# Kernel optimization log

Measured on AMD Instinct MI355X. Metric: run time of the kernel, lower is better.

Reference implementation:

```python
import jax, jax.numpy as jnp
import numpy as np

NUM_HEADS = 12
DILATIONS = (1, 2, 4)
POOL_STRIDE = 2
LINFORMER_SEQ = 128


def setup_inputs() -> dict:
    key = jax.random.key(0)
    ks = jax.random.split(key, 8)
    B, N, C = 32, 1024, 768
    bank = 64
    return {
        "x": jax.random.normal(ks[0], (B, N, C), jnp.float32),
        "Wqkv": jax.random.normal(ks[1], (C, 3 * C), jnp.float32) * 0.02,
        "bqkv": jnp.zeros((3 * C,), jnp.float32),
        "E_k": jax.random.normal(ks[2], (LINFORMER_SEQ, 64), jnp.float32) * 0.02,
        "E_v": jax.random.normal(ks[3], (LINFORMER_SEQ, 64), jnp.float32) * 0.02,
        "Wproj": jax.random.normal(ks[4], (C, C), jnp.float32) * 0.02,
        "bproj": jnp.zeros((C,), jnp.float32),
        "k_bank": jax.random.normal(ks[5], (B, bank, C), jnp.float32),
        "v_bank": jax.random.normal(ks[6], (B, bank, C), jnp.float32),
    }


def reference(x, Wqkv, bqkv, E_k, E_v, Wproj, bproj, k_bank, v_bank):
    B, N, C = x.shape
    H = NUM_HEADS
    D = C // H
    S = int(np.sqrt(N))  # spatial side, N must be a perfect square

    # multi-scale dilated token gather
    xg = x.reshape(B, S, S, C)
    multi = [xg[:, ::d, ::d, :].reshape(B, -1, C) for d in DILATIONS]
    xm = jnp.concatenate(multi, axis=1)  # (B, NM, C)

    # landmark average pooling (kernel=stride=POOL_STRIDE, no padding)
    NM = xm.shape[1]
    NP = NM // POOL_STRIDE
    xp = xm[:, : NP * POOL_STRIDE].reshape(B, NP, POOL_STRIDE, C).mean(axis=2)

    # qkv on pooled landmarks, keep k and v heads
    qkv_p = (xp @ Wqkv + bqkv).reshape(B, NP, 3, H, D)
    k = qkv_p[:, :, 1].transpose(0, 2, 1, 3)  # (B,H,NP,D)
    v = qkv_p[:, :, 2].transpose(0, 2, 1, 3)

    # truncate/pad to Linformer seq_len (here NP=672 > 128 -> truncate)
    if k.shape[2] < LINFORMER_SEQ:
        pad = LINFORMER_SEQ - k.shape[2]
        k = jnp.pad(k, ((0, 0), (0, 0), (0, pad), (0, 0)))
        v = jnp.pad(v, ((0, 0), (0, 0), (0, pad), (0, 0)))
    else:
        k = k[:, :, :LINFORMER_SEQ]
        v = v[:, :, :LINFORMER_SEQ]

    # Linformer low-rank compression: E.T @ k
    kc = jnp.einsum('sc,bhsd->bhcd', E_k, k)  # (B,H,64,D)
    vc = jnp.einsum('sc,bhsd->bhcd', E_v, v)

    # memory bank heads
    kb = k_bank.reshape(B, -1, H, D).transpose(0, 2, 1, 3)
    vb = v_bank.reshape(B, -1, H, D).transpose(0, 2, 1, 3)
    k_full = jnp.concatenate([kc, kb], axis=2)  # (B,H,128,D)
    v_full = jnp.concatenate([vc, vb], axis=2)

    # queries from full-resolution tokens
    q = (x @ Wqkv + bqkv).reshape(B, N, 3, H, D)[:, :, 0].transpose(0, 2, 1, 3)

    # scaled dot-product attention (dropout p=0 in eval / reference)
    scale = 1.0 / jnp.sqrt(jnp.asarray(D, x.dtype))
    scores = jnp.einsum('bhqd,bhkd->bhqk', q, k_full) * scale
    attn = jax.nn.softmax(scores, axis=-1)
    out = jnp.einsum('bhqk,bhkd->bhqd', attn, v_full)

    out = out.transpose(0, 2, 1, 3).reshape(B, N, C)
    return out @ Wproj + bproj
```

## Files before the change

kernel.cpp:

```cpp
#include <hip/hip_runtime.h>

#define BB    32
#define NSEQ  1024
#define CDIM  768
#define NH    12
#define HD    64
#define LKEYS 128
#define NPOOL 128

typedef __bf16 bf16x8 __attribute__((ext_vector_type(8)));
typedef float  f32x4  __attribute__((ext_vector_type(4)));

__device__ __forceinline__ ushort f2bf(float f) {
    union { float f; uint u; } v; v.f = f;
    uint u = v.u;
    uint r = u + 0x7FFFu + ((u >> 16) & 1u);
    return (ushort)(r >> 16);
}
__device__ __forceinline__ uint pack2(float x, float y) {
    return (uint)f2bf(x) | ((uint)f2bf(y) << 16);
}

__global__ __launch_bounds__(256) void cvt_bf16_kernel(const float* __restrict__ src,
                                                       ushort* __restrict__ dst, int n8)
{
    int idx = blockIdx.x * 256 + threadIdx.x;
    if (idx >= n8) return;
    float4 a = ((const float4*)src)[idx * 2];
    float4 b = ((const float4*)src)[idx * 2 + 1];
    uint4 o;
    o.x = pack2(a.x, a.y); o.y = pack2(a.z, a.w);
    o.z = pack2(b.x, b.y); o.w = pack2(b.z, b.w);
    ((uint4*)dst)[idx] = o;
}

__global__ __launch_bounds__(256) void transpose_cvt_kernel(const float* __restrict__ src,
                                                            ushort* __restrict__ dst,
                                                            int R, int C)
{
    __shared__ ushort tile[32][33];
    int bc = blockIdx.x * 32, br = blockIdx.y * 32;
    int tx = threadIdx.x & 31, ty = threadIdx.x >> 5;
#pragma unroll
    for (int i = 0; i < 32; i += 8)
        tile[ty + i][tx] = f2bf(src[(size_t)(br + ty + i) * C + bc + tx]);
    __syncthreads();
#pragma unroll
    for (int i = 0; i < 32; i += 8)
        dst[(size_t)(bc + ty + i) * R + br + tx] = tile[tx][ty + i];
}

__global__ __launch_bounds__(256) void pool_kernel(const float* __restrict__ x,
                                                   ushort* __restrict__ xp)
{
    int idx = blockIdx.x * 256 + threadIdx.x;
    int c8 = idx % 96;
    int t  = idx / 96;
    int i  = t % NPOOL;
    int b  = t / NPOOL;
    if (b >= BB) return;
    const float4* x4 = (const float4*)x;
    size_t base0 = ((size_t)(b * NSEQ + 2 * i)) * 192 + c8 * 2;
    size_t base1 = base0 + 192;
    float4 a0 = x4[base0], a1 = x4[base0 + 1];
    float4 b0 = x4[base1], b1 = x4[base1 + 1];
    uint4 o;
    o.x = pack2(0.5f * (a0.x + b0.x), 0.5f * (a0.y + b0.y));
    o.y = pack2(0.5f * (a0.z + b0.z), 0.5f * (a0.w + b0.w));
    o.z = pack2(0.5f * (a1.x + b1.x), 0.5f * (a1.y + b1.y));
    o.w = pack2(0.5f * (a1.z + b1.z), 0.5f * (a1.w + b1.w));
    ((uint4*)xp)[idx] = o;
}

template <bool OBF16>
__global__ __launch_bounds__(256) void mfma_gemm_kernel(
    const ushort* __restrict__ A, const ushort* __restrict__ Bt,
    const float* __restrict__ bias, void* __restrict__ Cout,
    int M, int N, int K)
{
    __shared__ ushort As[128 * 32];
    __shared__ ushort Bs[128 * 32];

    int tid  = threadIdx.x;
    int wave = tid >> 6, lane = tid & 63;

    int nwg  = gridDim.x * gridDim.y;
    int bid  = blockIdx.y * gridDim.x + blockIdx.x;
    int q    = nwg >> 3, r = nwg & 7;
    int xcd  = bid & 7, j = bid >> 3;
    int flat = (xcd < r ? xcd * (q + 1) : r * (q + 1) + (xcd - r) * q) + j;
    int n0 = (flat % gridDim.x) * 128;
    int m0 = (flat / gridDim.x) * 128;

    int wm = wave >> 1, wn = wave & 1;
    int lm = lane & 15, lh = lane >> 4;

    f32x4 acc[4][4] = {};

    for (int k0 = 0; k0 < K; k0 += 32) {
        __syncthreads();
#pragma unroll
        for (int t = 0; t < 2; t++) {
            int fl = wave * 128 + t * 64 + lane;
            int row = fl >> 2, kc = (fl & 3) * 8;
            const ushort* gA = A  + (size_t)(m0 + row) * K + k0 + kc;
            const ushort* gB = Bt + (size_t)(n0 + row) * K + k0 + kc;
            __builtin_amdgcn_global_load_lds(
                (const __attribute__((address_space(1))) void*)gA,
                (__attribute__((address_space(3))) void*)(As + (size_t)(wave * 128 + t * 64) * 8),
                16, 0, 0);
            __builtin_amdgcn_global_load_lds(
                (const __attribute__((address_space(1))) void*)gB,
                (__attribute__((address_space(3))) void*)(Bs + (size_t)(wave * 128 + t * 64) * 8),
                16, 0, 0);
        }
        __syncthreads();

        bf16x8 af[4], bfr[4];
#pragma unroll
        for (int i = 0; i < 4; i++)
            af[i] = *(const bf16x8*)((const void*)&As[(wm * 64 + i * 16 + lm) * 32 + lh * 8]);
#pragma unroll
        for (int jj = 0; jj < 4; jj++)
            bfr[jj] = *(const bf16x8*)((const void*)&Bs[(wn * 64 + jj * 16 + lm) * 32 + lh * 8]);
#pragma unroll
        for (int i = 0; i < 4; i++)
#pragma unroll
            for (int jj = 0; jj < 4; jj++)
                acc[i][jj] = __builtin_amdgcn_mfma_f32_16x16x32_bf16(af[i], bfr[jj], acc[i][jj], 0, 0, 0);
    }

    int crow = m0 + wm * 64, ccol = n0 + wn * 64;
#pragma unroll
    for (int jj = 0; jj < 4; jj++) {
        int col = ccol + jj * 16 + lm;
        float bb = bias[col];
        if constexpr (OBF16) {
            ushort* C = (ushort*)Cout;
#pragma unroll
            for (int i = 0; i < 4; i++)
#pragma unroll
                for (int rr = 0; rr < 4; rr++)
                    C[(size_t)(crow + i * 16 + lh * 4 + rr) * N + col] = f2bf(acc[i][jj][rr] + bb);
        } else {
            float* C = (float*)Cout;
#pragma unroll
            for (int i = 0; i < 4; i++)
#pragma unroll
                for (int rr = 0; rr < 4; rr++)
                    C[(size_t)(crow + i * 16 + lh * 4 + rr) * N + col] = acc[i][jj][rr] + bb;
        }
    }
}

__global__ __launch_bounds__(256) void compress_kernel(
    const float* __restrict__ kvp,
    const float* __restrict__ Ek, const float* __restrict__ Ev,
    const float* __restrict__ kbank, const float* __restrict__ vbank,
    ushort* __restrict__ kfull, ushort* __restrict__ vfullT)
{
    __shared__ float Es[128 * 64];
    __shared__ float Sl[128 * 64];

    int tid = threadIdx.x;
    int h = blockIdx.x, b = blockIdx.y, which = blockIdx.z;
    const float* E    = which ? Ev : Ek;
    const float* bank = which ? vbank : kbank;

#pragma unroll
    for (int i = 0; i < 8; i++) {
        int flat = tid + i * 256;
        *(float4*)&Es[flat * 4] = *(const float4*)&E[flat * 4];
    }
    const float* src = kvp + (size_t)b * 128 * 1536 + which * 768 + h * HD;
#pragma unroll
    for (int i = 0; i < 8; i++) {
        int flat = tid + i * 256;
        int s = flat >> 4, d4 = flat & 15;
        *(float4*)&Sl[s * 64 + d4 * 4] = *(const float4*)&src[(size_t)s * 1536 + d4 * 4];
    }

    const float* bankbase = bank + (size_t)b * 64 * CDIM + h * HD;
    ushort* outK = kfull  + (size_t)(b * NH + h) * LKEYS * HD;
    ushort* outV = vfullT + (size_t)(b * NH + h) * HD * LKEYS;

#pragma unroll
    for (int i = 0; i < 4; i++) {
        int flat = tid + i * 256;
        int j = flat >> 4, d4 = flat & 15;
        float4 v = *(const float4*)&bankbase[(size_t)j * CDIM + d4 * 4];
        if (!which) {
            ushort4 o;
            o.x = f2bf(v.x); o.y = f2bf(v.y); o.z = f2bf(v.z); o.w = f2bf(v.w);
            *(ushort4*)&outK[(size_t)(64 + j) * HD + d4 * 4] = o;
        } else {
            outV[(size_t)(d4 * 4 + 0) * LKEYS + 64 + j] = f2bf(v.x);
            outV[(size_t)(d4 * 4 + 1) * LKEYS + 64 + j] = f2bf(v.y);
            outV[(size_t)(d4 * 4 + 2) * LKEYS + 64 + j] = f2bf(v.z);
            outV[(size_t)(d4 * 4 + 3) * LKEYS + 64 + j] = f2bf(v.w);
        }
    }
    __syncthreads();

    int tx = tid & 15, ty = tid >> 4;
    float acc[4][4];
#pragma unroll
    for (int i = 0; i < 4; i++)
#pragma unroll
        for (int j = 0; j < 4; j++) acc[i][j] = 0.f;

#pragma unroll 4
    for (int s = 0; s < 128; s++) {
        float4 av = *(const float4*)&Es[s * 64 + ty * 4];
        float4 bv = *(const float4*)&Sl[s * 64 + tx * 4];
        float a[4] = {av.x, av.y, av.z, av.w};
        float bb[4] = {bv.x, bv.y, bv.z, bv.w};
#pragma unroll
        for (int i = 0; i < 4; i++)
#pragma unroll
            for (int j = 0; j < 4; j++)
                acc[i][j] += a[i] * bb[j];
    }
    if (!which) {
#pragma unroll
        for (int i = 0; i < 4; i++) {
            ushort4 o;
            o.x = f2bf(acc[i][0]); o.y = f2bf(acc[i][1]);
            o.z = f2bf(acc[i][2]); o.w = f2bf(acc[i][3]);
            *(ushort4*)&outK[(size_t)(ty * 4 + i) * HD + tx * 4] = o;
        }
    } else {
#pragma unroll
        for (int i = 0; i < 4; i++)
#pragma unroll
            for (int j = 0; j < 4; j++)
                outV[(size_t)(tx * 4 + j) * LKEYS + ty * 4 + i] = f2bf(acc[i][j]);
    }
}

__global__ __launch_bounds__(256) void attn_mfma_kernel(
    const ushort* __restrict__ qb, const ushort* __restrict__ kf,
    const ushort* __restrict__ vt, ushort* __restrict__ ob)
{
    __shared__ __align__(16) ushort lds[64 * 72 + 128 * 72 + 64 * 136];
    ushort* Qs = lds;
    ushort* Ks = lds + 64 * 72;
    ushort* Vs = lds + 64 * 72 + 128 * 72;
    ushort* Ps = lds;

    int tid  = threadIdx.x;
    int wave = tid >> 6, lane = tid & 63;
    int lm = lane & 15, lh = lane >> 4;
    int qt = blockIdx.x, h = blockIdx.y, b = blockIdx.z;

    const ushort* qbase = qb + ((size_t)(b * NSEQ + qt * 64)) * CDIM + h * HD;
    const ushort* kbase = kf + (size_t)(b * NH + h) * LKEYS * HD;
    const ushort* vbase = vt + (size_t)(b * NH + h) * HD * LKEYS;

#pragma unroll
    for (int it = 0; it < 2; it++) {
        int flat = tid + it * 256;
        int row = flat >> 3, seg = flat & 7;
        *(uint4*)&Qs[row * 72 + seg * 8] = *(const uint4*)&qbase[(size_t)row * CDIM + seg * 8];
    }
#pragma unroll
    for (int it = 0; it < 4; it++) {
        int flat = tid + it * 256;
        int row = flat >> 3, seg = flat & 7;
        *(uint4*)&Ks[row * 72 + seg * 8] = *(const uint4*)&kbase[(size_t)row * HD + seg * 8];
    }
#pragma unroll
    for (int it = 0; it < 4; it++) {
        int flat = tid + it * 256;
        int row = flat >> 4, seg = flat & 15;
        *(uint4*)&Vs[row * 136 + seg * 8] = *(const uint4*)&vbase[(size_t)row * LKEYS + seg * 8];
    }
    __syncthreads();

    f32x4 sacc[8] = {};
    bf16x8 aq[2];
#pragma unroll
    for (int ks = 0; ks < 2; ks++)
        aq[ks] = *(const bf16x8*)((const void*)&Qs[(wave * 16 + lm) * 72 + ks * 32 + lh * 8]);
#pragma unroll
    for (int j = 0; j < 8; j++)
#pragma unroll
        for (int ks = 0; ks < 2; ks++) {
            bf16x8 bk = *(const bf16x8*)((const void*)&Ks[(j * 16 + lm) * 72 + ks * 32 + lh * 8]);
            sacc[j] = __builtin_amdgcn_mfma_f32_16x16x32_bf16(aq[ks], bk, sacc[j], 0, 0, 0);
        }

    float rinv[4];
#pragma unroll
    for (int r = 0; r < 4; r++) {
        float m = sacc[0][r];
#pragma unroll
        for (int j = 1; j < 8; j++) m = fmaxf(m, sacc[j][r]);
#pragma unroll
        for (int off = 1; off < 16; off <<= 1) m = fmaxf(m, __shfl_xor(m, off, 64));
        float s = 0.f;
#pragma unroll
        for (int j = 0; j < 8; j++) {
            float e = __expf((sacc[j][r] - m) * 0.125f);
            sacc[j][r] = e;
            s += e;
        }
#pragma unroll
        for (int off = 1; off < 16; off <<= 1) s += __shfl_xor(s, off, 64);
        rinv[r] = 1.f / s;
    }

    __syncthreads();
#pragma unroll
    for (int j = 0; j < 8; j++)
#pragma unroll
        for (int r = 0; r < 4; r++)
            Ps[(size_t)(wave * 16 + lh * 4 + r) * 136 + j * 16 + lm] = f2bf(sacc[j][r] * rinv[r]);
    __syncthreads();

    f32x4 oacc[4] = {};
#pragma unroll
    for (int ks = 0; ks < 4; ks++) {
        bf16x8 ap = *(const bf16x8*)((const void*)&Ps[(wave * 16 + lm) * 136 + ks * 32 + lh * 8]);
#pragma unroll
        for (int j = 0; j < 4; j++) {
            bf16x8 bv = *(const bf16x8*)((const void*)&Vs[(j * 16 + lm) * 136 + ks * 32 + lh * 8]);
            oacc[j] = __builtin_amdgcn_mfma_f32_16x16x32_bf16(ap, bv, oacc[j], 0, 0, 0);
        }
    }

    ushort* obase = ob + ((size_t)(b * NSEQ + qt * 64)) * CDIM + h * HD;
#pragma unroll
    for (int j = 0; j < 4; j++)
#pragma unroll
        for (int r = 0; r < 4; r++)
            obase[(size_t)(wave * 16 + lh * 4 + r) * CDIM + j * 16 + lm] = f2bf(oacc[j][r]);
}

extern "C" void kernel_launch(void* const* d_in, const int* in_sizes, int n_in,
                              void* d_out, int out_size, void* d_ws, size_t ws_size,
                              hipStream_t stream)
{
    const float* x     = (const float*)d_in[0];
    const float* Wqkv  = (const float*)d_in[1];
    const float* bqkv  = (const float*)d_in[2];
    const float* Ek    = (const float*)d_in[3];
    const float* Ev    = (const float*)d_in[4];
    const float* Wproj = (const float*)d_in[5];
    const float* bproj = (const float*)d_in[6];
    const float* kbank = (const float*)d_in[7];
    const float* vbank = (const float*)d_in[8];
    float* out = (float*)d_out;
    float* ws  = (float*)d_ws;

    float*  kvp    = ws;
    ushort* qb_bf  = (ushort*)ws;
    ushort* x_bf   = (ushort*)(ws + 12582912);
    ushort* aob    = x_bf;
    ushort* xp_bf  = (ushort*)(ws + 25165824);
    ushort* Wq_t   = (ushort*)(ws + 26738688);
    ushort* Wp_t   = (ushort*)(ws + 27623424);
    ushort* k_full = (ushort*)(ws + 27918336);
    ushort* v_fullT= (ushort*)(ws + 29491200);

    cvt_bf16_kernel<<<12288, 256, 0, stream>>>(x, x_bf, 3145728);
    transpose_cvt_kernel<<<dim3(72, 24), 256, 0, stream>>>(Wqkv, Wq_t, CDIM, 3 * CDIM);
    transpose_cvt_kernel<<<dim3(24, 24), 256, 0, stream>>>(Wproj, Wp_t, CDIM, CDIM);
    pool_kernel<<<1536, 256, 0, stream>>>(x, xp_bf);

    mfma_gemm_kernel<false><<<dim3(12, 32), 256, 0, stream>>>(
        xp_bf, Wq_t + (size_t)CDIM * CDIM, bqkv + CDIM, kvp, 4096, 2 * CDIM, CDIM);
    compress_kernel<<<dim3(NH, BB, 2), 256, 0, stream>>>(
        kvp, Ek, Ev, kbank, vbank, k_full, v_fullT);

    mfma_gemm_kernel<true><<<dim3(6, 256), 256, 0, stream>>>(
        x_bf, Wq_t, bqkv, qb_bf, BB * NSEQ, CDIM, CDIM);

    attn_mfma_kernel<<<dim3(16, NH, BB), 256, 0, stream>>>(qb_bf, k_full, v_fullT, aob);

    mfma_gemm_kernel<false><<<dim3(6, 256), 256, 0, stream>>>(
        aob, Wp_t, bproj, out, BB * NSEQ, CDIM, CDIM);
}
```

Baseline: 394.2 us.

## Add 256x256-tile 4-stage pipelined GEMM for Q and output projections

Introduces a new GEMM kernel with 256x256 tiles, 512 threads and a 4-slot LDS ring filled by direct global-to-LDS loads with XOR swizzling, split A/B staging across the half-iterations, and explicit vmcnt waits. It also remaps block IDs so neighbouring tiles land on the same XCD. The two large M=32768 projection GEMMs use it instead of the older 128-tile kernel. The aim is more data reuse per tile, overlap of loads with MFMA work and better L2 locality, at the cost of fewer blocks (384) and heavy register and LDS use per block.

```diff
diff --git a/kernel.cpp b/kernel.cpp
--- a/kernel.cpp
+++ b/kernel.cpp
@@ -153,6 +153,145 @@
     }
 }
 
+template <bool OBF16>
+__global__ __launch_bounds__(512) void gemm256_kernel(
+    const ushort* __restrict__ A, const ushort* __restrict__ Bt,
+    const float* __restrict__ bias, void* __restrict__ Cout,
+    int M, int N, int K)
+{
+    __shared__ ushort As[4][256 * 32];
+    __shared__ ushort Bs[4][256 * 32];
+
+    int tid  = threadIdx.x;
+    int lane = tid & 63;
+    int wave = tid >> 6;
+
+    int nwg  = gridDim.x * gridDim.y;
+    int bid  = blockIdx.y * gridDim.x + blockIdx.x;
+    int q    = nwg >> 3, r = nwg & 7;
+    int xcd  = bid & 7, j = bid >> 3;
+    int flat = (xcd < r ? xcd * (q + 1) : r * (q + 1) + (xcd - r) * q) + j;
+    int n0 = (flat % gridDim.x) * 256;
+    int m0 = (flat / gridDim.x) * 256;
+
+    int wm = wave >> 2, wn = wave & 3;
+    int lm = lane & 15, lh = lane >> 4;
+
+    int NT = K >> 5;
+
+    auto stageA = [&](int tt) {
+        int slot = tt & 3;
+#pragma unroll
+        for (int ld = 0; ld < 2; ld++) {
+            int fl = ld * 512 + tid;
+            int prow = fl >> 2, pch = fl & 3;
+            int lch  = pch ^ ((prow >> 1) & 3);
+            const ushort* g = A + (size_t)(m0 + prow) * K + tt * 32 + lch * 8;
+            __builtin_amdgcn_global_load_lds(
+                (const __attribute__((address_space(1))) void*)g,
+                (__attribute__((address_space(3))) void*)(&As[slot][fl * 8]),
+                16, 0, 0);
+        }
+    };
+    auto stageB = [&](int tt) {
+        int slot = tt & 3;
+#pragma unroll
+        for (int ld = 0; ld < 2; ld++) {
+            int fl = ld * 512 + tid;
+            int prow = fl >> 2, pch = fl & 3;
+            int lch  = pch ^ ((prow >> 1) & 3);
+            const ushort* g = Bt + (size_t)(n0 + prow) * K + tt * 32 + lch * 8;
+            __builtin_amdgcn_global_load_lds(
+                (const __attribute__((address_space(1))) void*)g,
+                (__attribute__((address_space(3))) void*)(&Bs[slot][fl * 8]),
+                16, 0, 0);
+        }
+    };
+
+    f32x4 acc[8][4] = {};
+
+    stageA(0); stageB(0);
+    stageA(1); stageB(1);
+    stageA(2); stageB(2);
+
+    for (int t = 0; t < NT; t++) {
+        int slot = t & 3;
+
+        if (t + 3 < NT) stageA(t + 3);
+
+        if (t + 3 < NT)       asm volatile("s_waitcnt vmcnt(10)" ::: "memory");
+        else if (t + 3 == NT) asm volatile("s_waitcnt vmcnt(8)"  ::: "memory");
+        else if (t + 2 == NT) asm volatile("s_waitcnt vmcnt(4)"  ::: "memory");
+        else                  asm volatile("s_waitcnt vmcnt(0)"  ::: "memory");
+        __builtin_amdgcn_s_barrier();
+        asm volatile("" ::: "memory");
+
+        bf16x8 bfrag[4], afrag[4];
+#pragma unroll
+        for (int jj = 0; jj < 4; jj++) {
+            int rn = wn * 64 + jj * 16 + lm;
+            int pch = lh ^ ((rn >> 1) & 3);
+            bfrag[jj] = *(const bf16x8*)((const void*)&Bs[slot][rn * 32 + pch * 8]);
+        }
+#pragma unroll
+        for (int i = 0; i < 4; i++) {
+            int rm = wm * 128 + i * 16 + lm;
+            int pch = lh ^ ((rm >> 1) & 3);
+            afrag[i] = *(const bf16x8*)((const void*)&As[slot][rm * 32 + pch * 8]);
+        }
+        __builtin_amdgcn_s_setprio(1);
+#pragma unroll
+        for (int i = 0; i < 4; i++)
+#pragma unroll
+            for (int jj = 0; jj < 4; jj++)
+                acc[i][jj] = __builtin_amdgcn_mfma_f32_16x16x32_bf16(afrag[i], bfrag[jj], acc[i][jj], 0, 0, 0);
+        __builtin_amdgcn_s_setprio(0);
+        __builtin_amdgcn_s_barrier();
+
+        if (t + 3 < NT) stageB(t + 3);
+#pragma unroll
+        for (int i = 0; i < 4; i++) {
+            int rm = wm * 128 + 64 + i * 16 + lm;
+            int pch = lh ^ ((rm >> 1) & 3);
+            afrag[i] = *(const bf16x8*)((const void*)&As[slot][rm * 32 + pch * 8]);
+        }
+        __builtin_amdgcn_s_setprio(1);
+#pragma unroll
+        for (int i = 0; i < 4; i++)
+#pragma unroll
+            for (int jj = 0; jj < 4; jj++)
+                acc[4 + i][jj] = __builtin_amdgcn_mfma_f32_16x16x32_bf16(afrag[i], bfrag[jj], acc[4 + i][jj], 0, 0, 0);
+        __builtin_amdgcn_s_setprio(0);
+        __builtin_amdgcn_s_barrier();
+    }
+
+    int crow = m0 + wm * 128, ccol = n0 + wn * 64;
+#pragma unroll
+    for (int jj = 0; jj < 4; jj++) {
+        int col = ccol + jj * 16 + lm;
+        float bb = bias[col];
+        if constexpr (OBF16) {
+            ushort* C = (ushort*)Cout;
+#pragma unroll
+            for (int i = 0; i < 8; i++) {
+                int rowb = crow + (i >> 2) * 64 + (i & 3) * 16 + lh * 4;
+#pragma unroll
+                for (int rr = 0; rr < 4; rr++)
+                    C[(size_t)(rowb + rr) * N + col] = f2bf(acc[i][jj][rr] + bb);
+            }
+        } else {
+            float* C = (float*)Cout;
+#pragma unroll
+            for (int i = 0; i < 8; i++) {
+                int rowb = crow + (i >> 2) * 64 + (i & 3) * 16 + lh * 4;
+#pragma unroll
+                for (int rr = 0; rr < 4; rr++)
+                    C[(size_t)(rowb + rr) * N + col] = acc[i][jj][rr] + bb;
+            }
+        }
+    }
+}
+
 __global__ __launch_bounds__(256) void compress_kernel(
     const float* __restrict__ kvp,
     const float* __restrict__ Ek, const float* __restrict__ Ev,
@@ -373,11 +512,11 @@
     compress_kernel<<<dim3(NH, BB, 2), 256, 0, stream>>>(
         kvp, Ek, Ev, kbank, vbank, k_full, v_fullT);
 
-    mfma_gemm_kernel<true><<<dim3(6, 256), 256, 0, stream>>>(
+    gemm256_kernel<true><<<dim3(3, 128), 512, 0, stream>>>(
         x_bf, Wq_t, bqkv, qb_bf, BB * NSEQ, CDIM, CDIM);
 
     attn_mfma_kernel<<<dim3(16, NH, BB), 256, 0, stream>>>(qb_bf, k_full, v_fullT, aob);
 
-    mfma_gemm_kernel<false><<<dim3(6, 256), 256, 0, stream>>>(
+    gemm256_kernel<false><<<dim3(3, 128), 512, 0, stream>>>(
         aob, Wp_t, bproj, out, BB * NSEQ, CDIM, CDIM);
 }
```

After: 443.9 us. +12.6%, slower.
